# Kernel tuning notes

Measured on AMD Instinct MI355X. Metric: run time of the kernel, lower is better.

## Reference

```python
import jax, jax.numpy as jnp
import numpy as np

N_NODES = 200000
N_EDGES = 600000
NODE_IN = 32
EDGE_IN = 16
HID = 128
L = 3
MLP_HID = 128
LN_EPS = 1e-5


def _dense(k, fan_in, fan_out):
    kw, kb = jax.random.split(k)
    s = 1.0 / np.sqrt(fan_in)
    W = jax.random.uniform(kw, (fan_in, fan_out), jnp.float32, -s, s)
    b = jax.random.uniform(kb, (fan_out,), jnp.float32, -s, s)
    return W, b


def setup_inputs() -> dict:
    key = jax.random.key(0)
    ks = jax.random.split(key, 16)
    x = jax.random.normal(ks[0], (N_NODES, NODE_IN), jnp.float32)
    edge_index = jax.random.randint(ks[1], (2, N_EDGES), 0, N_NODES, jnp.int32)
    edge_attr = jax.random.normal(ks[2], (N_EDGES, EDGE_IN), jnp.float32)
    enc_w, enc_b = _dense(ks[3], NODE_IN, HID)
    ee_w, ee_b = _dense(ks[4], EDGE_IN, HID)
    w1s, b1s, w2s, b2s = [], [], [], []
    for i in range(L):
        W1, B1 = _dense(jax.random.fold_in(ks[5], i), HID, HID)
        W2, B2 = _dense(jax.random.fold_in(ks[6], i), HID, HID)
        w1s.append(W1); b1s.append(B1); w2s.append(W2); b2s.append(B2)
    gine_w1 = jnp.stack(w1s); gine_b1 = jnp.stack(b1s)
    gine_w2 = jnp.stack(w2s); gine_b2 = jnp.stack(b2s)
    gine_eps = jnp.zeros((L,), jnp.float32)  # PyG GINEConv default eps=0
    ln_g = jnp.ones((L, HID), jnp.float32)
    ln_b = jnp.zeros((L, HID), jnp.float32)
    mlp_w1, mlp_b1 = _dense(ks[7], 3 * HID, MLP_HID)
    mlp_w2, mlp_b2 = _dense(ks[8], MLP_HID, 1)
    return {"x": x, "edge_index": edge_index, "edge_attr": edge_attr,
            "enc_w": enc_w, "enc_b": enc_b, "ee_w": ee_w, "ee_b": ee_b,
            "gine_w1": gine_w1, "gine_b1": gine_b1, "gine_w2": gine_w2,
            "gine_b2": gine_b2, "gine_eps": gine_eps, "ln_g": ln_g, "ln_b": ln_b,
            "mlp_w1": mlp_w1, "mlp_b1": mlp_b1, "mlp_w2": mlp_w2, "mlp_b2": mlp_b2}


def reference(x, edge_index, edge_attr, enc_w, enc_b, ee_w, ee_b,
              gine_w1, gine_b1, gine_w2, gine_b2, gine_eps, ln_g, ln_b,
              mlp_w1, mlp_b1, mlp_w2, mlp_b2):
    src, dst = edge_index[0], edge_index[1]
    h = x @ enc_w + enc_b                      # [N, HID]
    e = edge_attr @ ee_w + ee_b                # [E, HID]
    for i in range(L):
        # GINEConv: out = MLP((1+eps)*x + sum_{j->i} relu(x_j + e_ji))
        msg = jax.nn.relu(h[src] + e)          # [E, HID] gather+fuse
        agg = jax.ops.segment_sum(msg, dst, num_segments=N_NODES)
        z = (1.0 + gine_eps[i]) * h + agg
        z = jax.nn.relu(z @ gine_w1[i] + gine_b1[i]) @ gine_w2[i] + gine_b2[i]
        # PyG LayerNorm (default mode='graph'): normalize over all nodes+features
        mu = jnp.mean(z)
        zc = z - mu
        var = jnp.mean(zc * zc)
        z = zc / jnp.sqrt(var + LN_EPS) * ln_g[i] + ln_b[i]
        h = jax.nn.relu(z)                     # dropout is identity at inference
    edge_inputs = jnp.concatenate([h[src], h[dst], e], axis=1)  # [E, 3*HID]
    hmid = jax.nn.relu(edge_inputs @ mlp_w1 + mlp_b1)
    logits = (hmid @ mlp_w2 + mlp_b2)[:, 0]    # [E]
    return logits
```

## Files before the change

### kernel.cpp

```cpp
#include <hip/hip_runtime.h>
#include <hip/hip_bf16.h>

#define N_NODES 200000
#define N_EDGES 600000
#define NODE_IN 32
#define EDGE_IN 16
#define HID     128
#define LN_EPS  1e-5f
#define SCAN_B  512
#define NBLK_SCAN 391

typedef __attribute__((ext_vector_type(8))) short short8;
typedef __attribute__((ext_vector_type(4))) float f32x4;

static __device__ __forceinline__ ushort f2b(float f) {
    unsigned u = __builtin_bit_cast(unsigned, f);
    unsigned r = (u + 0x7fffu + ((u >> 16) & 1u)) >> 16;
    return (ushort)r;
}
static __device__ __forceinline__ float b2f(ushort us) {
    unsigned u = ((unsigned)us) << 16;
    return __builtin_bit_cast(float, u);
}

__global__ __launch_bounds__(256) void k_csr_zero(int* __restrict__ deg)
{
    const int i = blockIdx.x * 256 + threadIdx.x;
    if (i < N_NODES) deg[i] = 0;
}

__global__ __launch_bounds__(256) void k_csr_deg(
    const int* __restrict__ ei, int* __restrict__ deg)
{
    const int e = blockIdx.x * 256 + threadIdx.x;
    if (e < N_EDGES) atomicAdd(&deg[ei[N_EDGES + e]], 1);
}

__global__ __launch_bounds__(SCAN_B) void k_scan1(
    const int* __restrict__ deg, int* __restrict__ part)
{
    __shared__ int s[SCAN_B];
    const int t = threadIdx.x, i = blockIdx.x * SCAN_B + t;
    s[t] = (i < N_NODES) ? deg[i] : 0;
    __syncthreads();
    for (int off = SCAN_B / 2; off; off >>= 1) {
        if (t < off) s[t] += s[t + off];
        __syncthreads();
    }
    if (t == 0) part[blockIdx.x] = s[0];
}

__global__ void k_scan2(int* __restrict__ part, int* __restrict__ rowptr)
{
    if (threadIdx.x == 0) {
        int run = 0;
        for (int b = 0; b < NBLK_SCAN; b++) { int x = part[b]; part[b] = run; run += x; }
        rowptr[N_NODES] = N_EDGES;
    }
}

__global__ __launch_bounds__(SCAN_B) void k_scan3(
    const int* __restrict__ deg, const int* __restrict__ part,
    int* __restrict__ rowptr, int* __restrict__ cursor)
{
    __shared__ int s[SCAN_B];
    const int t = threadIdx.x, i = blockIdx.x * SCAN_B + t;
    const int v = (i < N_NODES) ? deg[i] : 0;
    s[t] = v;
    __syncthreads();
    for (int off = 1; off < SCAN_B; off <<= 1) {
        int x = (t >= off) ? s[t - off] : 0;
        __syncthreads();
        s[t] += x;
        __syncthreads();
    }
    if (i < N_NODES) {
        const int ex = s[t] - v + part[blockIdx.x];
        rowptr[i] = ex;
        cursor[i] = ex;
    }
}

__global__ __launch_bounds__(256) void k_csr_fill(
    const int* __restrict__ ei, int* __restrict__ cursor, int* __restrict__ eid)
{
    const int e = blockIdx.x * 256 + threadIdx.x;
    if (e < N_EDGES) {
        const int slot = atomicAdd(&cursor[ei[N_EDGES + e]], 1);
        eid[slot] = e;
    }
}

__global__ __launch_bounds__(256) void k_prep_g(
    const float* __restrict__ gw1, const float* __restrict__ gw2,
    ushort* __restrict__ wpk)
{
    const int gidx = blockIdx.x * 256 + threadIdx.x;
    const int m    = gidx >> 11;
    const int r    = gidx & 2047;
    const int lane = r & 63;
    const int ntkb = r >> 6;
    const int nt = ntkb & 7, kb = ntkb >> 3;
    const int n  = nt * 16 + (lane & 15);
    const int k0 = kb * 32 + (lane >> 4) * 8;
    const float* W = (m < 3) ? gw1 + (size_t)m * HID * HID
                             : gw2 + (size_t)(m - 3) * HID * HID;
    short8 v;
#pragma unroll
    for (int j = 0; j < 8; j++)
        v[j] = (short)f2b(W[(size_t)(k0 + j) * HID + n]);
    ((short8*)wpk)[gidx] = v;
}

__global__ __launch_bounds__(256) void k_prep_m(
    const float* __restrict__ mw1, ushort* __restrict__ w1p)
{
    const int gidx = blockIdx.x * 256 + threadIdx.x;
    const int lane = gidx & 63;
    const int ntkb = gidx >> 6;
    const int nt = ntkb & 7, kb = ntkb >> 3;
    const int n  = nt * 16 + (lane & 15);
    const int k0 = kb * 32 + (lane >> 4) * 8;
    short8 v;
#pragma unroll
    for (int j = 0; j < 8; j++)
        v[j] = (short)f2b(mw1[(size_t)(k0 + j) * HID + n]);
    ((short8*)w1p)[gidx] = v;
}

__global__ __launch_bounds__(256) void k_node_enc(
    const float* __restrict__ x, const float* __restrict__ w,
    const float* __restrict__ b, const float* __restrict__ epsp,
    ushort* __restrict__ hb, float* __restrict__ agg,
    float* __restrict__ red)
{
    __shared__ float sx[16][NODE_IN];
    const int tid = threadIdx.x;
    const int n0  = blockIdx.x * 16;
    float* sxf = &sx[0][0];
    sxf[tid]       = x[(size_t)n0 * NODE_IN + tid];
    sxf[tid + 256] = x[(size_t)n0 * NODE_IN + tid + 256];

    const int f   = tid & 127;
    const int grp = tid >> 7;
    float wcol[NODE_IN];
#pragma unroll
    for (int k = 0; k < NODE_IN; k++) wcol[k] = w[k * HID + f];
    const float bf = b[f];
    const float alpha = 1.0f + epsp[0];
    __syncthreads();

#pragma unroll
    for (int it = 0; it < 8; it++) {
        const int ln = it * 2 + grp;
        const int n  = n0 + ln;
        const float4* sx4 = (const float4*)sx[ln];
        float acc = bf;
#pragma unroll
        for (int k4 = 0; k4 < NODE_IN / 4; k4++) {
            float4 v = sx4[k4];
            acc += v.x * wcol[k4*4] + v.y * wcol[k4*4+1] +
                   v.z * wcol[k4*4+2] + v.w * wcol[k4*4+3];
        }
        hb[(size_t)n * HID + f]  = f2b(acc);
        agg[(size_t)n * HID + f] = alpha * acc;
    }
    if (blockIdx.x == 0 && tid == 0) { red[0] = 0.f; red[1] = 0.f; }
}

__global__ __launch_bounds__(256) void k_agg(
    const ushort* __restrict__ hb, const int* __restrict__ ei,
    const float* __restrict__ ea, const float* __restrict__ eew,
    const float* __restrict__ eeb,
    const int* __restrict__ rowptr, const int* __restrict__ eid,
    float* __restrict__ agg)
{
    const int tid = threadIdx.x;
    const int n   = blockIdx.x * 2 + (tid >> 7);
    const int f   = tid & 127;
    const int* __restrict__ src = ei;

    float wcol[EDGE_IN];
#pragma unroll
    for (int k = 0; k < EDGE_IN; k++) wcol[k] = eew[k * HID + f];
    const float bf = eeb[f];

    float s = 0.f;
    const int beg = rowptr[n], end = rowptr[n + 1];
    for (int j = beg; j < end; j++) {
        const int e  = eid[j];
        const int sn = src[e];
        const float4* ea4 = (const float4*)(ea + (size_t)e * EDGE_IN);
        float4 a0 = ea4[0], a1 = ea4[1], a2 = ea4[2], a3 = ea4[3];
        float ev = bf;
        ev += a0.x*wcol[0]  + a0.y*wcol[1]  + a0.z*wcol[2]  + a0.w*wcol[3];
        ev += a1.x*wcol[4]  + a1.y*wcol[5]  + a1.z*wcol[6]  + a1.w*wcol[7];
        ev += a2.x*wcol[8]  + a2.y*wcol[9]  + a2.z*wcol[10] + a2.w*wcol[11];
        ev += a3.x*wcol[12] + a3.y*wcol[13] + a3.z*wcol[14] + a3.w*wcol[15];
        s += fmaxf(b2f(hb[(size_t)sn * HID + f]) + ev, 0.f);
    }
    agg[(size_t)n * HID + f] += s;
}

template<bool IN_BF16, bool RELU_OUT, bool REDUCE>
__global__ __launch_bounds__(256) void k_gemm(
    const void* in_, const short8* __restrict__ wp,
    const float* __restrict__ bias, ushort* out, float* __restrict__ red)
{
    __shared__ ushort sU[64][136];
    const int tid = threadIdx.x;
    const int m0  = blockIdx.x * 64;

    if constexpr (IN_BF16) {
        const short8* in8 = (const short8*)((const ushort*)in_ + (size_t)m0 * HID);
#pragma unroll
        for (int it = 0; it < 4; it++) {
            const int q = it * 256 + tid;
            const int r = q >> 4, c8 = q & 15;
            *(short8*)&sU[r][c8 * 8] = in8[q];
        }
    } else {
        const float4* in4 = (const float4*)((const float*)in_ + (size_t)m0 * HID);
#pragma unroll
        for (int it = 0; it < 8; it++) {
            const int q = it * 256 + tid;
            const int r = q >> 5, c4 = q & 31;
            float4 v = in4[q];
            ushort4 u;
            u.x = f2b(v.x); u.y = f2b(v.y); u.z = f2b(v.z); u.w = f2b(v.w);
            *(ushort4*)&sU[r][c4 * 4] = u;
        }
    }
    __syncthreads();

    const int lane = tid & 63;
    const int r0   = (tid >> 6) * 16;
    const int arow = r0 + (lane & 15);
    const int kg8  = (lane >> 4) * 8;
    f32x4 acc[8] = {};
    for (int kb = 0; kb < 4; kb++) {
        short8 af = *(const short8*)&sU[arow][kb * 32 + kg8];
#pragma unroll
        for (int nt = 0; nt < 8; nt++) {
            short8 bf8 = wp[(kb * 8 + nt) * 64 + lane];
            acc[nt] = __builtin_amdgcn_mfma_f32_16x16x32_bf16(af, bf8, acc[nt], 0, 0, 0);
        }
    }

    float lsum = 0.f, lsq = 0.f;
    const int rowb = m0 + r0 + (lane >> 4) * 4;
#pragma unroll
    for (int nt = 0; nt < 8; nt++) {
        const int c = nt * 16 + (lane & 15);
        const float bc = bias[c];
#pragma unroll
        for (int j = 0; j < 4; j++) {
            float o = acc[nt][j] + bc;
            if constexpr (RELU_OUT) o = fmaxf(o, 0.f);
            if constexpr (REDUCE) { lsum += o; lsq += o * o; }
            out[(size_t)(rowb + j) * HID + c] = f2b(o);
        }
    }

    if constexpr (REDUCE) {
#pragma unroll
        for (int off = 32; off; off >>= 1) {
            lsum += __shfl_down(lsum, off);
            lsq  += __shfl_down(lsq, off);
        }
        __shared__ float sws[4], swq[4];
        const int wid = tid >> 6;
        if ((tid & 63) == 0) { sws[wid] = lsum; swq[wid] = lsq; }
        __syncthreads();
        if (tid == 0) {
            atomicAdd(&red[0], sws[0] + sws[1] + sws[2] + sws[3]);
            atomicAdd(&red[1], swq[0] + swq[1] + swq[2] + swq[3]);
        }
    }
}

__global__ void k_lnfin(float* __restrict__ red)
{
    if (threadIdx.x == 0) {
        const float inv = 1.0f / ((float)N_NODES * (float)HID);
        const float mu  = red[0] * inv;
        const float var = red[1] * inv - mu * mu;
        red[2] = mu;
        red[3] = 1.0f / sqrtf(var + LN_EPS);
        red[0] = 0.f; red[1] = 0.f;
    }
}

template<bool FUSE_NEXT>
__global__ __launch_bounds__(256) void k_ln(
    ushort* zh, const float* __restrict__ red,
    const float* __restrict__ g, const float* __restrict__ b,
    const float* __restrict__ eps_next, float* __restrict__ agg)
{
    const float mu = red[2], rstd = red[3];
    const int i = blockIdx.x * 256 + threadIdx.x;
    short8 z8 = ((const short8*)zh)[i];
    const int cb = (i & 15) * 2;
    float4 g0 = ((const float4*)g)[cb],  g1 = ((const float4*)g)[cb + 1];
    float4 b0 = ((const float4*)b)[cb],  b1 = ((const float4*)b)[cb + 1];
    float o[8];
    o[0] = fmaxf((b2f((ushort)z8[0]) - mu) * rstd * g0.x + b0.x, 0.f);
    o[1] = fmaxf((b2f((ushort)z8[1]) - mu) * rstd * g0.y + b0.y, 0.f);
    o[2] = fmaxf((b2f((ushort)z8[2]) - mu) * rstd * g0.z + b0.z, 0.f);
    o[3] = fmaxf((b2f((ushort)z8[3]) - mu) * rstd * g0.w + b0.w, 0.f);
    o[4] = fmaxf((b2f((ushort)z8[4]) - mu) * rstd * g1.x + b1.x, 0.f);
    o[5] = fmaxf((b2f((ushort)z8[5]) - mu) * rstd * g1.y + b1.y, 0.f);
    o[6] = fmaxf((b2f((ushort)z8[6]) - mu) * rstd * g1.z + b1.z, 0.f);
    o[7] = fmaxf((b2f((ushort)z8[7]) - mu) * rstd * g1.w + b1.w, 0.f);
    short8 h8;
#pragma unroll
    for (int j = 0; j < 8; j++) h8[j] = (short)f2b(o[j]);
    ((short8*)zh)[i] = h8;
    if constexpr (FUSE_NEXT) {
        const float a = 1.0f + eps_next[0];
        float4 A0, A1;
        A0.x = a*o[0]; A0.y = a*o[1]; A0.z = a*o[2]; A0.w = a*o[3];
        A1.x = a*o[4]; A1.y = a*o[5]; A1.z = a*o[6]; A1.w = a*o[7];
        ((float4*)agg)[i * 2]     = A0;
        ((float4*)agg)[i * 2 + 1] = A1;
    }
}

__global__ __launch_bounds__(256) void k_mlp(
    const ushort* __restrict__ hb, const int* __restrict__ ei,
    const float* __restrict__ ea, const float* __restrict__ eew,
    const float* __restrict__ eeb,
    const ushort* __restrict__ w1p, const float* __restrict__ b1,
    const float* __restrict__ w2, const float* __restrict__ b2,
    float* __restrict__ out)
{
    __shared__ ushort sE[64][136];
    const int* __restrict__ src = ei;
    const int* __restrict__ dst = ei + N_EDGES;
    const int tid = threadIdx.x;
    const int e0  = blockIdx.x * 64;
    const int lane = tid & 63;
    const int wv   = tid >> 6;
    const int r0   = wv * 16;

    {
        const int f = tid & 127;
        float wcol[EDGE_IN];
#pragma unroll
        for (int k = 0; k < EDGE_IN; k++) wcol[k] = eew[k * HID + f];
        const float bf = eeb[f];
#pragma unroll
        for (int it = 0; it < 32; it++) {
            const int e = it * 2 + (tid >> 7);
            const float4* ea4 = (const float4*)(ea + (size_t)(e0 + e) * EDGE_IN);
            float ev = bf;
#pragma unroll
            for (int k4 = 0; k4 < EDGE_IN / 4; k4++) {
                float4 v = ea4[k4];
                ev += v.x * wcol[k4*4] + v.y * wcol[k4*4+1] +
                      v.z * wcol[k4*4+2] + v.w * wcol[k4*4+3];
            }
            sE[e][f] = f2b(ev);
        }
    }

    const int er = e0 + r0 + (lane & 15);
    const int kg = lane >> 4;
    const int ns = src[er], nd = dst[er];
    const short8* hb8 = (const short8*)hb;
    short8 af[8];
#pragma unroll
    for (int kb = 0; kb < 4; kb++) af[kb]     = hb8[(size_t)ns * 16 + kb * 4 + kg];
#pragma unroll
    for (int kb = 0; kb < 4; kb++) af[4 + kb] = hb8[(size_t)nd * 16 + kb * 4 + kg];
    __syncthreads();

    f32x4 acc[8] = {};
    const short8* bfr = (const short8*)w1p;
#pragma unroll
    for (int kb = 0; kb < 8; kb++) {
#pragma unroll
        for (int nt = 0; nt < 8; nt++) {
            short8 bfrag = bfr[(kb * 8 + nt) * 64 + lane];
            acc[nt] = __builtin_amdgcn_mfma_f32_16x16x32_bf16(af[kb], bfrag, acc[nt], 0, 0, 0);
        }
    }
#pragma unroll
    for (int kb = 8; kb < 12; kb++) {
        short8 ae = *(const short8*)&sE[r0 + (lane & 15)][(kb - 8) * 32 + kg * 8];
#pragma unroll
        for (int nt = 0; nt < 8; nt++) {
            short8 bfrag = bfr[(kb * 8 + nt) * 64 + lane];
            acc[nt] = __builtin_amdgcn_mfma_f32_16x16x32_bf16(ae, bfrag, acc[nt], 0, 0, 0);
        }
    }

    float s0 = 0.f, s1 = 0.f, s2 = 0.f, s3 = 0.f;
#pragma unroll
    for (int nt = 0; nt < 8; nt++) {
        const int col = nt * 16 + (lane & 15);
        const float b1c = b1[col];
        const float w2c = w2[col];
        s0 += fmaxf(acc[nt][0] + b1c, 0.f) * w2c;
        s1 += fmaxf(acc[nt][1] + b1c, 0.f) * w2c;
        s2 += fmaxf(acc[nt][2] + b1c, 0.f) * w2c;
        s3 += fmaxf(acc[nt][3] + b1c, 0.f) * w2c;
    }
#pragma unroll
    for (int m = 1; m < 16; m <<= 1) {
        s0 += __shfl_xor(s0, m); s1 += __shfl_xor(s1, m);
        s2 += __shfl_xor(s2, m); s3 += __shfl_xor(s3, m);
    }
    if ((lane & 15) == 0) {
        const float bb = b2[0];
        const int eb = e0 + r0 + kg * 4;
        out[eb + 0] = s0 + bb; out[eb + 1] = s1 + bb;
        out[eb + 2] = s2 + bb; out[eb + 3] = s3 + bb;
    }
}

extern "C" void kernel_launch(void* const* d_in, const int* in_sizes, int n_in,
                              void* d_out, int out_size, void* d_ws, size_t ws_size,
                              hipStream_t stream)
{
    const float* x    = (const float*)d_in[0];
    const int*   ei   = (const int*)  d_in[1];
    const float* ea   = (const float*)d_in[2];
    const float* encw = (const float*)d_in[3];
    const float* encb = (const float*)d_in[4];
    const float* eew  = (const float*)d_in[5];
    const float* eeb  = (const float*)d_in[6];
    const float* gw1  = (const float*)d_in[7];
    const float* gb1  = (const float*)d_in[8];
    const float* gw2  = (const float*)d_in[9];
    const float* gb2  = (const float*)d_in[10];
    const float* geps = (const float*)d_in[11];
    const float* lng  = (const float*)d_in[12];
    const float* lnb  = (const float*)d_in[13];
    const float* mw1  = (const float*)d_in[14];
    const float* mb1  = (const float*)d_in[15];
    const float* mw2  = (const float*)d_in[16];
    const float* mb2  = (const float*)d_in[17];

    float* ws = (float*)d_ws;
    const size_t NH = (size_t)N_NODES * HID;
    float*  agg = ws;
    ushort* zh  = (ushort*)(ws + NH);
    int*    csr = (int*)(ws + NH + NH / 2);
    float*  red = ws + 2 * NH;

    int* deg    = csr;
    int* rowptr = csr + 200000;
    int* cursor = csr + 400064;
    int* eid    = csr + 600064;
    int* part   = csr + 1200064;

    ushort* wpk = (ushort*)d_out;

    k_prep_g<<<48, 256, 0, stream>>>(gw1, gw2, wpk);
    k_csr_zero<<<(N_NODES + 255) / 256, 256, 0, stream>>>(deg);
    k_csr_deg<<<(N_EDGES + 255) / 256, 256, 0, stream>>>(ei, deg);
    k_scan1<<<NBLK_SCAN, SCAN_B, 0, stream>>>(deg, part);
    k_scan2<<<1, 64, 0, stream>>>(part, rowptr);
    k_scan3<<<NBLK_SCAN, SCAN_B, 0, stream>>>(deg, part, rowptr, cursor);
    k_csr_fill<<<(N_EDGES + 255) / 256, 256, 0, stream>>>(ei, cursor, eid);
    k_node_enc<<<N_NODES / 16, 256, 0, stream>>>(x, encw, encb, geps, zh, agg, red);

    const int LN_BLKS = (int)(NH / 8 / 256);
    for (int l = 0; l < 3; l++) {
        k_agg<<<N_NODES / 2, 256, 0, stream>>>(zh, ei, ea, eew, eeb,
                                               rowptr, eid, agg);
        k_gemm<false, true, false><<<N_NODES / 64, 256, 0, stream>>>(
            agg, (const short8*)wpk + (size_t)l * 2048,
            gb1 + (size_t)l * HID, zh, nullptr);
        k_gemm<true, false, true><<<N_NODES / 64, 256, 0, stream>>>(
            zh, (const short8*)wpk + (size_t)(3 + l) * 2048,
            gb2 + (size_t)l * HID, zh, red);
        k_lnfin<<<1, 64, 0, stream>>>(red);
        if (l < 2)
            k_ln<true><<<LN_BLKS, 256, 0, stream>>>(
                zh, red, lng + (size_t)l * HID, lnb + (size_t)l * HID,
                geps + l + 1, agg);
        else
            k_ln<false><<<LN_BLKS, 256, 0, stream>>>(
                zh, red, lng + (size_t)l * HID, lnb + (size_t)l * HID,
                nullptr, nullptr);
    }

    ushort* w1p = (ushort*)agg;
    k_prep_m<<<24, 256, 0, stream>>>(mw1, w1p);
    k_mlp<<<N_EDGES / 64, 256, 0, stream>>>(zh, ei, ea, eew, eeb,
                                            w1p, mb1, mw2, mb2, (float*)d_out);
}
```

Before: 1.793 ms.

## Fuse neighbor aggregation with first GIN MLP GEMM using LDS tile accumulation

Replaces the per-node aggregation kernel and the first GEMM with one kernel. Each block owns 64 destination nodes, seeds an LDS tile with (1+eps)*h, scatters edge messages into it with shared-memory atomics, then runs the MFMA GEMM straight from LDS. This drops the fp32 agg buffer's global write and read and its initialization in the encoder and LN kernels, and separates the h and z buffers. In exchange it adds LDS atomic contention and loses parallelism, since each block walks all edges of its 64 nodes with only 4 waves and 2 features per lane.

```diff
diff --git a/kernel.cpp b/kernel.cpp
--- a/kernel.cpp
+++ b/kernel.cpp
@@ -130,8 +130,7 @@
 
 __global__ __launch_bounds__(256) void k_node_enc(
     const float* __restrict__ x, const float* __restrict__ w,
-    const float* __restrict__ b, const float* __restrict__ epsp,
-    ushort* __restrict__ hb, float* __restrict__ agg,
+    const float* __restrict__ b, ushort* __restrict__ hb,
     float* __restrict__ red)
 {
     __shared__ float sx[16][NODE_IN];
@@ -147,7 +146,6 @@
 #pragma unroll
     for (int k = 0; k < NODE_IN; k++) wcol[k] = w[k * HID + f];
     const float bf = b[f];
-    const float alpha = 1.0f + epsp[0];
     __syncthreads();
 
 #pragma unroll
@@ -162,44 +160,97 @@
             acc += v.x * wcol[k4*4] + v.y * wcol[k4*4+1] +
                    v.z * wcol[k4*4+2] + v.w * wcol[k4*4+3];
         }
-        hb[(size_t)n * HID + f]  = f2b(acc);
-        agg[(size_t)n * HID + f] = alpha * acc;
+        hb[(size_t)n * HID + f] = f2b(acc);
     }
     if (blockIdx.x == 0 && tid == 0) { red[0] = 0.f; red[1] = 0.f; }
 }
 
-__global__ __launch_bounds__(256) void k_agg(
+__global__ __launch_bounds__(256) void k_ag1(
     const ushort* __restrict__ hb, const int* __restrict__ ei,
     const float* __restrict__ ea, const float* __restrict__ eew,
-    const float* __restrict__ eeb,
+    const float* __restrict__ eeb, const float* __restrict__ epsp,
     const int* __restrict__ rowptr, const int* __restrict__ eid,
-    float* __restrict__ agg)
-{
+    const short8* __restrict__ wp, const float* __restrict__ bias,
+    ushort* __restrict__ z)
+{
+    __shared__ float sZ[64][132];
     const int tid = threadIdx.x;
-    const int n   = blockIdx.x * 2 + (tid >> 7);
-    const int f   = tid & 127;
-    const int* __restrict__ src = ei;
-
-    float wcol[EDGE_IN];
-#pragma unroll
-    for (int k = 0; k < EDGE_IN; k++) wcol[k] = eew[k * HID + f];
-    const float bf = eeb[f];
-
-    float s = 0.f;
-    const int beg = rowptr[n], end = rowptr[n + 1];
-    for (int j = beg; j < end; j++) {
+    const int n0  = blockIdx.x * 64;
+    const float alpha = 1.0f + epsp[0];
+
+    const short8* hb8 = (const short8*)(hb + (size_t)n0 * HID);
+#pragma unroll
+    for (int it = 0; it < 4; it++) {
+        const int q = it * 256 + tid;
+        const int r = q >> 4, c8 = q & 15;
+        short8 v = hb8[q];
+#pragma unroll
+        for (int j = 0; j < 8; j++)
+            sZ[r][c8 * 8 + j] = alpha * b2f((ushort)v[j]);
+    }
+    __syncthreads();
+
+    const int lane = tid & 63;
+    const int wv   = tid >> 6;
+    const int f0   = lane * 2;
+    float2 wc[EDGE_IN];
+#pragma unroll
+    for (int k = 0; k < EDGE_IN; k++) {
+        wc[k].x = eew[k * HID + f0];
+        wc[k].y = eew[k * HID + f0 + 1];
+    }
+    const float bf0 = eeb[f0], bf1 = eeb[f0 + 1];
+
+    const int jbeg = rowptr[n0], jend = rowptr[n0 + 64];
+    for (int j = jbeg + wv; j < jend; j += 4) {
         const int e  = eid[j];
-        const int sn = src[e];
+        const int sn = ei[e];
+        const int dl = ei[N_EDGES + e] - n0;
+        const unsigned hv = *(const unsigned*)(hb + (size_t)sn * HID + f0);
+        const float h0 = b2f((ushort)(hv & 0xffffu));
+        const float h1 = b2f((ushort)(hv >> 16));
         const float4* ea4 = (const float4*)(ea + (size_t)e * EDGE_IN);
         float4 a0 = ea4[0], a1 = ea4[1], a2 = ea4[2], a3 = ea4[3];
-        float ev = bf;
-        ev += a0.x*wcol[0]  + a0.y*wcol[1]  + a0.z*wcol[2]  + a0.w*wcol[3];
-        ev += a1.x*wcol[4]  + a1.y*wcol[5]  + a1.z*wcol[6]  + a1.w*wcol[7];
-        ev += a2.x*wcol[8]  + a2.y*wcol[9]  + a2.z*wcol[10] + a2.w*wcol[11];
-        ev += a3.x*wcol[12] + a3.y*wcol[13] + a3.z*wcol[14] + a3.w*wcol[15];
-        s += fmaxf(b2f(hb[(size_t)sn * HID + f]) + ev, 0.f);
-    }
-    agg[(size_t)n * HID + f] += s;
+        float ev0 = bf0 + a0.x*wc[0].x + a0.y*wc[1].x + a0.z*wc[2].x + a0.w*wc[3].x
+                        + a1.x*wc[4].x + a1.y*wc[5].x + a1.z*wc[6].x + a1.w*wc[7].x
+                        + a2.x*wc[8].x + a2.y*wc[9].x + a2.z*wc[10].x + a2.w*wc[11].x
+                        + a3.x*wc[12].x + a3.y*wc[13].x + a3.z*wc[14].x + a3.w*wc[15].x;
+        float ev1 = bf1 + a0.x*wc[0].y + a0.y*wc[1].y + a0.z*wc[2].y + a0.w*wc[3].y
+                        + a1.x*wc[4].y + a1.y*wc[5].y + a1.z*wc[6].y + a1.w*wc[7].y
+                        + a2.x*wc[8].y + a2.y*wc[9].y + a2.z*wc[10].y + a2.w*wc[11].y
+                        + a3.x*wc[12].y + a3.y*wc[13].y + a3.z*wc[14].y + a3.w*wc[15].y;
+        atomicAdd(&sZ[dl][f0],     fmaxf(h0 + ev0, 0.f));
+        atomicAdd(&sZ[dl][f0 + 1], fmaxf(h1 + ev1, 0.f));
+    }
+    __syncthreads();
+
+    const int r0   = wv * 16;
+    const int arow = r0 + (lane & 15);
+    const int kg8  = (lane >> 4) * 8;
+    f32x4 acc[8] = {};
+    for (int kb = 0; kb < 4; kb++) {
+        short8 af;
+#pragma unroll
+        for (int j = 0; j < 8; j++)
+            af[j] = (short)f2b(sZ[arow][kb * 32 + kg8 + j]);
+#pragma unroll
+        for (int nt = 0; nt < 8; nt++) {
+            short8 bf8 = wp[(kb * 8 + nt) * 64 + lane];
+            acc[nt] = __builtin_amdgcn_mfma_f32_16x16x32_bf16(af, bf8, acc[nt], 0, 0, 0);
+        }
+    }
+
+    const int rowb = n0 + r0 + (lane >> 4) * 4;
+#pragma unroll
+    for (int nt = 0; nt < 8; nt++) {
+        const int c = nt * 16 + (lane & 15);
+        const float bc = bias[c];
+#pragma unroll
+        for (int j = 0; j < 4; j++) {
+            float o = fmaxf(acc[nt][j] + bc, 0.f);
+            z[(size_t)(rowb + j) * HID + c] = f2b(o);
+        }
+    }
 }
 
 template<bool IN_BF16, bool RELU_OUT, bool REDUCE>
@@ -291,39 +342,27 @@
     }
 }
 
-template<bool FUSE_NEXT>
 __global__ __launch_bounds__(256) void k_ln(
-    ushort* zh, const float* __restrict__ red,
+    const ushort* __restrict__ z, const float* __restrict__ red,
     const float* __restrict__ g, const float* __restrict__ b,
-    const float* __restrict__ eps_next, float* __restrict__ agg)
+    ushort* __restrict__ hb)
 {
     const float mu = red[2], rstd = red[3];
     const int i = blockIdx.x * 256 + threadIdx.x;
-    short8 z8 = ((const short8*)zh)[i];
+    short8 z8 = ((const short8*)z)[i];
     const int cb = (i & 15) * 2;
     float4 g0 = ((const float4*)g)[cb],  g1 = ((const float4*)g)[cb + 1];
     float4 b0 = ((const float4*)b)[cb],  b1 = ((const float4*)b)[cb + 1];
-    float o[8];
-    o[0] = fmaxf((b2f((ushort)z8[0]) - mu) * rstd * g0.x + b0.x, 0.f);
-    o[1] = fmaxf((b2f((ushort)z8[1]) - mu) * rstd * g0.y + b0.y, 0.f);
-    o[2] = fmaxf((b2f((ushort)z8[2]) - mu) * rstd * g0.z + b0.z, 0.f);
-    o[3] = fmaxf((b2f((ushort)z8[3]) - mu) * rstd * g0.w + b0.w, 0.f);
-    o[4] = fmaxf((b2f((ushort)z8[4]) - mu) * rstd * g1.x + b1.x, 0.f);
-    o[5] = fmaxf((b2f((ushort)z8[5]) - mu) * rstd * g1.y + b1.y, 0.f);
-    o[6] = fmaxf((b2f((ushort)z8[6]) - mu) * rstd * g1.z + b1.z, 0.f);
-    o[7] = fmaxf((b2f((ushort)z8[7]) - mu) * rstd * g1.w + b1.w, 0.f);
     short8 h8;
-#pragma unroll
-    for (int j = 0; j < 8; j++) h8[j] = (short)f2b(o[j]);
-    ((short8*)zh)[i] = h8;
-    if constexpr (FUSE_NEXT) {
-        const float a = 1.0f + eps_next[0];
-        float4 A0, A1;
-        A0.x = a*o[0]; A0.y = a*o[1]; A0.z = a*o[2]; A0.w = a*o[3];
-        A1.x = a*o[4]; A1.y = a*o[5]; A1.z = a*o[6]; A1.w = a*o[7];
-        ((float4*)agg)[i * 2]     = A0;
-        ((float4*)agg)[i * 2 + 1] = A1;
-    }
+    h8[0] = (short)f2b(fmaxf((b2f((ushort)z8[0]) - mu) * rstd * g0.x + b0.x, 0.f));
+    h8[1] = (short)f2b(fmaxf((b2f((ushort)z8[1]) - mu) * rstd * g0.y + b0.y, 0.f));
+    h8[2] = (short)f2b(fmaxf((b2f((ushort)z8[2]) - mu) * rstd * g0.z + b0.z, 0.f));
+    h8[3] = (short)f2b(fmaxf((b2f((ushort)z8[3]) - mu) * rstd * g0.w + b0.w, 0.f));
+    h8[4] = (short)f2b(fmaxf((b2f((ushort)z8[4]) - mu) * rstd * g1.x + b1.x, 0.f));
+    h8[5] = (short)f2b(fmaxf((b2f((ushort)z8[5]) - mu) * rstd * g1.y + b1.y, 0.f));
+    h8[6] = (short)f2b(fmaxf((b2f((ushort)z8[6]) - mu) * rstd * g1.z + b1.z, 0.f));
+    h8[7] = (short)f2b(fmaxf((b2f((ushort)z8[7]) - mu) * rstd * g1.w + b1.w, 0.f));
+    ((short8*)hb)[i] = h8;
 }
 
 __global__ __launch_bounds__(256) void k_mlp(
@@ -444,10 +483,12 @@
 
     float* ws = (float*)d_ws;
     const size_t NH = (size_t)N_NODES * HID;
-    float*  agg = ws;
-    ushort* zh  = (ushort*)(ws + NH);
-    int*    csr = (int*)(ws + NH + NH / 2);
-    float*  red = ws + 2 * NH;
+    ushort* hb  = (ushort*)ws;
+    ushort* z   = (ushort*)(ws + NH / 2);
+    int*    csr = (int*)(ws + NH);
+    float*  red = ws + NH + 1300000;
+    ushort* wpk = (ushort*)(ws + NH + 1300016);
+    ushort* w1p = (ushort*)(ws + NH + 1350000);
 
     int* deg    = csr;
     int* rowptr = csr + 200000;
@@ -455,40 +496,29 @@
     int* eid    = csr + 600064;
     int* part   = csr + 1200064;
 
-    ushort* wpk = (ushort*)d_out;
-
     k_prep_g<<<48, 256, 0, stream>>>(gw1, gw2, wpk);
+    k_prep_m<<<24, 256, 0, stream>>>(mw1, w1p);
     k_csr_zero<<<(N_NODES + 255) / 256, 256, 0, stream>>>(deg);
     k_csr_deg<<<(N_EDGES + 255) / 256, 256, 0, stream>>>(ei, deg);
     k_scan1<<<NBLK_SCAN, SCAN_B, 0, stream>>>(deg, part);
     k_scan2<<<1, 64, 0, stream>>>(part, rowptr);
     k_scan3<<<NBLK_SCAN, SCAN_B, 0, stream>>>(deg, part, rowptr, cursor);
     k_csr_fill<<<(N_EDGES + 255) / 256, 256, 0, stream>>>(ei, cursor, eid);
-    k_node_enc<<<N_NODES / 16, 256, 0, stream>>>(x, encw, encb, geps, zh, agg, red);
+    k_node_enc<<<N_NODES / 16, 256, 0, stream>>>(x, encw, encb, hb, red);
 
     const int LN_BLKS = (int)(NH / 8 / 256);
     for (int l = 0; l < 3; l++) {
-        k_agg<<<N_NODES / 2, 256, 0, stream>>>(zh, ei, ea, eew, eeb,
-                                               rowptr, eid, agg);
-        k_gemm<false, true, false><<<N_NODES / 64, 256, 0, stream>>>(
-            agg, (const short8*)wpk + (size_t)l * 2048,
-            gb1 + (size_t)l * HID, zh, nullptr);
+        k_ag1<<<N_NODES / 64, 256, 0, stream>>>(
+            hb, ei, ea, eew, eeb, geps + l, rowptr, eid,
+            (const short8*)wpk + (size_t)l * 2048, gb1 + (size_t)l * HID, z);
         k_gemm<true, false, true><<<N_NODES / 64, 256, 0, stream>>>(
-            zh, (const short8*)wpk + (size_t)(3 + l) * 2048,
-            gb2 + (size_t)l * HID, zh, red);
+            z, (const short8*)wpk + (size_t)(3 + l) * 2048,
+            gb2 + (size_t)l * HID, z, red);
         k_lnfin<<<1, 64, 0, stream>>>(red);
-        if (l < 2)
-            k_ln<true><<<LN_BLKS, 256, 0, stream>>>(
-                zh, red, lng + (size_t)l * HID, lnb + (size_t)l * HID,
-                geps + l + 1, agg);
-        else
-            k_ln<false><<<LN_BLKS, 256, 0, stream>>>(
-                zh, red, lng + (size_t)l * HID, lnb + (size_t)l * HID,
-                nullptr, nullptr);
-    }
-
-    ushort* w1p = (ushort*)agg;
-    k_prep_m<<<24, 256, 0, stream>>>(mw1, w1p);
-    k_mlp<<<N_EDGES / 64, 256, 0, stream>>>(zh, ei, ea, eew, eeb,
+        k_ln<<<LN_BLKS, 256, 0, stream>>>(
+            z, red, lng + (size_t)l * HID, lnb + (size_t)l * HID, hb);
+    }
+
+    k_mlp<<<N_EDGES / 64, 256, 0, stream>>>(hb, ei, ea, eew, eeb,
                                             w1p, mb1, mw2, mb2, (float*)d_out);
 }
```

Result: slower. 2.078 ms (+15.9%).

## Replace per-node CSR gather with edge-parallel sorted segmented atomic aggregation

Applied to the files above, without the earlier changes.

Aggregation changes from one block per destination node walking its CSR list to edge-parallel blocks over destination-sorted edges. Each thread accumulates runs of equal destination across 8 edges and flushes partial sums with atomicAdd. The CSR fill now writes permuted src, dst and edge_attr arrays so that reads in the message kernel are contiguous instead of going through eid indirection. The aim is to remove load imbalance from variable degree and the indirect loads, at the cost of float atomics, nondeterministic summation order, and extra workspace; the MLP weight prep is also moved into its own workspace buffer.

```diff
diff --git a/kernel.cpp b/kernel.cpp
--- a/kernel.cpp
+++ b/kernel.cpp
@@ -82,12 +82,19 @@
 }
 
 __global__ __launch_bounds__(256) void k_csr_fill(
-    const int* __restrict__ ei, int* __restrict__ cursor, int* __restrict__ eid)
+    const int* __restrict__ ei, const float* __restrict__ ea,
+    int* __restrict__ cursor, int* __restrict__ srcp,
+    int* __restrict__ dstp, float* __restrict__ eap)
 {
     const int e = blockIdx.x * 256 + threadIdx.x;
     if (e < N_EDGES) {
-        const int slot = atomicAdd(&cursor[ei[N_EDGES + e]], 1);
-        eid[slot] = e;
+        const int d = ei[N_EDGES + e];
+        const int slot = atomicAdd(&cursor[d], 1);
+        srcp[slot] = ei[e];
+        dstp[slot] = d;
+        const float4* s4 = (const float4*)(ea + (size_t)e * EDGE_IN);
+        float4* o4 = (float4*)(eap + (size_t)slot * EDGE_IN);
+        o4[0] = s4[0]; o4[1] = s4[1]; o4[2] = s4[2]; o4[3] = s4[3];
     }
 }
 
@@ -131,7 +138,7 @@
 __global__ __launch_bounds__(256) void k_node_enc(
     const float* __restrict__ x, const float* __restrict__ w,
     const float* __restrict__ b, const float* __restrict__ epsp,
-    ushort* __restrict__ hb, float* __restrict__ agg,
+    ushort* __restrict__ hz, float* __restrict__ agg,
     float* __restrict__ red)
 {
     __shared__ float sx[16][NODE_IN];
@@ -162,44 +169,50 @@
             acc += v.x * wcol[k4*4] + v.y * wcol[k4*4+1] +
                    v.z * wcol[k4*4+2] + v.w * wcol[k4*4+3];
         }
-        hb[(size_t)n * HID + f]  = f2b(acc);
+        hz[(size_t)n * HID + f]  = f2b(acc);
         agg[(size_t)n * HID + f] = alpha * acc;
     }
     if (blockIdx.x == 0 && tid == 0) { red[0] = 0.f; red[1] = 0.f; }
 }
 
-__global__ __launch_bounds__(256) void k_agg(
-    const ushort* __restrict__ hb, const int* __restrict__ ei,
-    const float* __restrict__ ea, const float* __restrict__ eew,
-    const float* __restrict__ eeb,
-    const int* __restrict__ rowptr, const int* __restrict__ eid,
+__global__ __launch_bounds__(256) void k_msg2(
+    const ushort* __restrict__ hz, const int* __restrict__ srcp,
+    const int* __restrict__ dstp, const float* __restrict__ eap,
+    const float* __restrict__ eew, const float* __restrict__ eeb,
     float* __restrict__ agg)
 {
     const int tid = threadIdx.x;
-    const int n   = blockIdx.x * 2 + (tid >> 7);
     const int f   = tid & 127;
-    const int* __restrict__ src = ei;
+    const int s0  = blockIdx.x * 16 + (tid >> 7) * 8;
 
     float wcol[EDGE_IN];
 #pragma unroll
     for (int k = 0; k < EDGE_IN; k++) wcol[k] = eew[k * HID + f];
     const float bf = eeb[f];
 
-    float s = 0.f;
-    const int beg = rowptr[n], end = rowptr[n + 1];
-    for (int j = beg; j < end; j++) {
-        const int e  = eid[j];
-        const int sn = src[e];
-        const float4* ea4 = (const float4*)(ea + (size_t)e * EDGE_IN);
-        float4 a0 = ea4[0], a1 = ea4[1], a2 = ea4[2], a3 = ea4[3];
+    int   prev = dstp[s0];
+    float sum  = 0.f;
+#pragma unroll
+    for (int it = 0; it < 8; it++) {
+        const int s  = s0 + it;
+        const int d  = dstp[s];
+        const int sn = srcp[s];
+        const float4* e4 = (const float4*)(eap + (size_t)s * EDGE_IN);
+        float4 a0 = e4[0], a1 = e4[1], a2 = e4[2], a3 = e4[3];
         float ev = bf;
         ev += a0.x*wcol[0]  + a0.y*wcol[1]  + a0.z*wcol[2]  + a0.w*wcol[3];
         ev += a1.x*wcol[4]  + a1.y*wcol[5]  + a1.z*wcol[6]  + a1.w*wcol[7];
         ev += a2.x*wcol[8]  + a2.y*wcol[9]  + a2.z*wcol[10] + a2.w*wcol[11];
         ev += a3.x*wcol[12] + a3.y*wcol[13] + a3.z*wcol[14] + a3.w*wcol[15];
-        s += fmaxf(b2f(hb[(size_t)sn * HID + f]) + ev, 0.f);
-    }
-    agg[(size_t)n * HID + f] += s;
+        const float m = fmaxf(b2f(hz[(size_t)sn * HID + f]) + ev, 0.f);
+        if (d != prev) {
+            atomicAdd(&agg[(size_t)prev * HID + f], sum);
+            prev = d; sum = m;
+        } else {
+            sum += m;
+        }
+    }
+    atomicAdd(&agg[(size_t)prev * HID + f], sum);
 }
 
 template<bool IN_BF16, bool RELU_OUT, bool REDUCE>
@@ -293,13 +306,13 @@
 
 template<bool FUSE_NEXT>
 __global__ __launch_bounds__(256) void k_ln(
-    ushort* zh, const float* __restrict__ red,
+    ushort* hz, const float* __restrict__ red,
     const float* __restrict__ g, const float* __restrict__ b,
     const float* __restrict__ eps_next, float* __restrict__ agg)
 {
     const float mu = red[2], rstd = red[3];
     const int i = blockIdx.x * 256 + threadIdx.x;
-    short8 z8 = ((const short8*)zh)[i];
+    short8 z8 = ((const short8*)hz)[i];
     const int cb = (i & 15) * 2;
     float4 g0 = ((const float4*)g)[cb],  g1 = ((const float4*)g)[cb + 1];
     float4 b0 = ((const float4*)b)[cb],  b1 = ((const float4*)b)[cb + 1];
@@ -315,7 +328,7 @@
     short8 h8;
 #pragma unroll
     for (int j = 0; j < 8; j++) h8[j] = (short)f2b(o[j]);
-    ((short8*)zh)[i] = h8;
+    ((short8*)hz)[i] = h8;
     if constexpr (FUSE_NEXT) {
         const float a = 1.0f + eps_next[0];
         float4 A0, A1;
@@ -327,7 +340,7 @@
 }
 
 __global__ __launch_bounds__(256) void k_mlp(
-    const ushort* __restrict__ hb, const int* __restrict__ ei,
+    const ushort* __restrict__ hz, const int* __restrict__ ei,
     const float* __restrict__ ea, const float* __restrict__ eew,
     const float* __restrict__ eeb,
     const ushort* __restrict__ w1p, const float* __restrict__ b1,
@@ -367,7 +380,7 @@
     const int er = e0 + r0 + (lane & 15);
     const int kg = lane >> 4;
     const int ns = src[er], nd = dst[er];
-    const short8* hb8 = (const short8*)hb;
+    const short8* hb8 = (const short8*)hz;
     short8 af[8];
 #pragma unroll
     for (int kb = 0; kb < 4; kb++) af[kb]     = hb8[(size_t)ns * 16 + kb * 4 + kg];
@@ -444,51 +457,51 @@
 
     float* ws = (float*)d_ws;
     const size_t NH = (size_t)N_NODES * HID;
-    float*  agg = ws;
-    ushort* zh  = (ushort*)(ws + NH);
-    int*    csr = (int*)(ws + NH + NH / 2);
-    float*  red = ws + 2 * NH;
-
-    int* deg    = csr;
-    int* rowptr = csr + 200000;
-    int* cursor = csr + 400064;
-    int* eid    = csr + 600064;
-    int* part   = csr + 1200064;
-
-    ushort* wpk = (ushort*)d_out;
+    float*  agg  = ws;
+    ushort* hz   = (ushort*)(ws + NH);
+    float*  eap  = ws + NH + NH / 2;
+    int*    srcp = (int*)(ws + 48000000);
+    int*    dstp = (int*)(ws + 48600000);
+    int*    deg  = (int*)(ws + 49200000);
+    int*    rowp = (int*)(ws + 49400000);
+    int*    curs = (int*)(ws + 49600064);
+    int*    part = (int*)(ws + 49800064);
+    float*  red  = ws + 49800640;
+    ushort* wpk  = (ushort*)(ws + 49800704);
+    ushort* w1p  = (ushort*)(ws + 49850000);
 
     k_prep_g<<<48, 256, 0, stream>>>(gw1, gw2, wpk);
+    k_prep_m<<<24, 256, 0, stream>>>(mw1, w1p);
     k_csr_zero<<<(N_NODES + 255) / 256, 256, 0, stream>>>(deg);
     k_csr_deg<<<(N_EDGES + 255) / 256, 256, 0, stream>>>(ei, deg);
     k_scan1<<<NBLK_SCAN, SCAN_B, 0, stream>>>(deg, part);
-    k_scan2<<<1, 64, 0, stream>>>(part, rowptr);
-    k_scan3<<<NBLK_SCAN, SCAN_B, 0, stream>>>(deg, part, rowptr, cursor);
-    k_csr_fill<<<(N_EDGES + 255) / 256, 256, 0, stream>>>(ei, cursor, eid);
-    k_node_enc<<<N_NODES / 16, 256, 0, stream>>>(x, encw, encb, geps, zh, agg, red);
+    k_scan2<<<1, 64, 0, stream>>>(part, rowp);
+    k_scan3<<<NBLK_SCAN, SCAN_B, 0, stream>>>(deg, part, rowp, curs);
+    k_csr_fill<<<(N_EDGES + 255) / 256, 256, 0, stream>>>(ei, ea, curs,
+                                                          srcp, dstp, eap);
+    k_node_enc<<<N_NODES / 16, 256, 0, stream>>>(x, encw, encb, geps, hz, agg, red);
 
     const int LN_BLKS = (int)(NH / 8 / 256);
     for (int l = 0; l < 3; l++) {
-        k_agg<<<N_NODES / 2, 256, 0, stream>>>(zh, ei, ea, eew, eeb,
-                                               rowptr, eid, agg);
+        k_msg2<<<N_EDGES / 16, 256, 0, stream>>>(hz, srcp, dstp, eap,
+                                                 eew, eeb, agg);
         k_gemm<false, true, false><<<N_NODES / 64, 256, 0, stream>>>(
             agg, (const short8*)wpk + (size_t)l * 2048,
-            gb1 + (size_t)l * HID, zh, nullptr);
+            gb1 + (size_t)l * HID, hz, nullptr);
         k_gemm<true, false, true><<<N_NODES / 64, 256, 0, stream>>>(
-            zh, (const short8*)wpk + (size_t)(3 + l) * 2048,
-            gb2 + (size_t)l * HID, zh, red);
+            hz, (const short8*)wpk + (size_t)(3 + l) * 2048,
+            gb2 + (size_t)l * HID, hz, red);
         k_lnfin<<<1, 64, 0, stream>>>(red);
         if (l < 2)
             k_ln<true><<<LN_BLKS, 256, 0, stream>>>(
-                zh, red, lng + (size_t)l * HID, lnb + (size_t)l * HID,
+                hz, red, lng + (size_t)l * HID, lnb + (size_t)l * HID,
                 geps + l + 1, agg);
         else
             k_ln<false><<<LN_BLKS, 256, 0, stream>>>(
-                zh, red, lng + (size_t)l * HID, lnb + (size_t)l * HID,
+                hz, red, lng + (size_t)l * HID, lnb + (size_t)l * HID,
                 nullptr, nullptr);
     }
 
-    ushort* w1p = (ushort*)agg;
-    k_prep_m<<<24, 256, 0, stream>>>(mw1, w1p);
-    k_mlp<<<N_EDGES / 64, 256, 0, stream>>>(zh, ei, ea, eew, eeb,
+    k_mlp<<<N_EDGES / 64, 256, 0, stream>>>(hz, ei, ea, eew, eeb,
                                             w1p, mb1, mw2, mb2, (float*)d_out);
 }
```

New measurement: 1.571 ms. 1.14x faster.
